# Kernel optimization log

Measured on AMD Instinct MI355X. Metric: run time of the kernel, lower is better.

Reference implementation:

```python
import jax, jax.numpy as jnp
import numpy as np

SIZE = 128   # feature dim
N = 4096     # number of mesh nodes


def setup_inputs() -> dict:
    key = jax.random.key(0)
    k_f, k_adj, k_q, k_k = jax.random.split(key, 4)
    # f: [size, N] node features (features-first, as in the torch module); scaled
    # so QK dot products stay O(1) and exp() is numerically safe.
    f = jax.random.normal(k_f, (SIZE, N), dtype=jnp.float32) * 0.1
    # neighbors: [N, N] binary adjacency with self-loops (every row sums > 0).
    adj = (jax.random.uniform(k_adj, (N, N)) < 0.005).astype(jnp.float32)
    neighbors = jnp.maximum(adj, jnp.eye(N, dtype=jnp.float32))
    # learned per-feature scale vectors (nn.init.normal_)
    wq = jax.random.normal(k_q, (SIZE,), dtype=jnp.float32)
    wk = jax.random.normal(k_k, (SIZE,), dtype=jnp.float32)
    return {"f": f, "neighbors": neighbors, "wq": wq, "wk": wk}


def reference(f, neighbors, wq, wk):
    # elementwise-scaled queries/keys: [size, N]
    wq_f = wq[:, None] * f
    wk_f = wk[:, None] * f
    # S[i, j] = exp(<wq_f[:, i], wk_f[:, j]>)  -> [N, N]
    S = jnp.exp(jnp.einsum('dn,dm->nm', wq_f, wk_f))
    # normalize by neighbor-sums: S / (neighbors @ S).T
    S = S / jnp.matmul(neighbors, S).T
    return S
```

## Files before the change

kernel.cpp:

```cpp
#include <hip/hip_runtime.h>
#include <hip/hip_fp16.h>

#define N     4096
#define SIZE  128
#define CAP   128
#define NMAX  120
#define RB    16
#define TB    1024

typedef __attribute__((ext_vector_type(8))) _Float16 f16x8;
typedef __attribute__((ext_vector_type(2))) __fp16 fp16x2;
typedef __attribute__((ext_vector_type(4))) float f32x4;

__device__ __forceinline__ unsigned int pk2(float lo, float hi) {
    union { fp16x2 v; unsigned int u; } c;
    c.v = __builtin_amdgcn_cvt_pkrtz(lo, hi);
    return c.u;
}
__device__ __forceinline__ __half2 u2h(unsigned int u) {
    union { unsigned int u; __half2 h; } c; c.u = u; return c.h;
}

__global__ __launch_bounds__(256)
void setup(const float* __restrict__ nb, const float* __restrict__ f,
           const float* __restrict__ wq, const float* __restrict__ wk,
           int* __restrict__ cnt, int* __restrict__ idx,
           _Float16* __restrict__ Af, _Float16* __restrict__ Bf) {
    __shared__ float sf[SIZE][16];
    __shared__ float sqw[SIZE];
    const int t = threadIdx.x;

    if (blockIdx.x < N / 4) {
        const int lane = t & 63;
        const int wv   = t >> 6;
        const int j    = blockIdx.x * 4 + wv;
        const float4* row4 = (const float4*)(nb + (size_t)j * N);
        int* irow = idx + (size_t)j * CAP;

        float4 v[16];
#pragma unroll
        for (int s = 0; s < 16; ++s) v[s] = row4[s * 64 + lane];

        unsigned long long m = 0ull;
#pragma unroll
        for (int s = 0; s < 16; ++s) {
            const float e[4] = {v[s].x, v[s].y, v[s].z, v[s].w};
#pragma unroll
            for (int q = 0; q < 4; ++q)
                if (e[q] != 0.0f) m |= 1ull << (s * 4 + q);
        }
        if (((j >> 2) & 63) == lane) m &= ~(1ull << ((j >> 8) * 4 + (j & 3)));

        const int pc = __popcll(m);
        int scan = pc;
#pragma unroll
        for (int s = 1; s < 64; s <<= 1) {
            const int o = __shfl_up(scan, s);
            if (lane >= s) scan += o;
        }
        int p = scan - pc;
        unsigned long long mm = m;
        while (mm) {
            const int b = __ffsll(mm) - 1;
            mm &= mm - 1ull;
            const int c = 4 * ((b >> 2) * 64 + lane) + (b & 3);
            if (p < NMAX) irow[p] = c;
            ++p;
        }
        if (lane == 63) {
            int n = scan;
            if (n > NMAX) n = NMAX;
            const int n8 = (n + 7) & ~7;
            for (int q = n; q < n8 + 8; ++q) irow[q] = N;
            cnt[j] = n8 >> 3;
        }
    } else {
        const int tile = blockIdx.x - N / 4;
        if (t < SIZE) sqw[t] = wq[t] * wk[t];
        const int col0 = t & 15;
#pragma unroll
        for (int it = 0; it < 8; ++it) {
            const int k = (t >> 4) + it * 16;
            sf[k][col0] = f[(size_t)k * N + tile * 16 + col0];
        }
        __syncthreads();
        const int ks   = t >> 6;
        const int lane = t & 63;
        const int quad = lane >> 4;
        const int col  = lane & 15;
        f16x8 va, vb;
#pragma unroll
        for (int jj = 0; jj < 8; ++jj) {
            const int k = ks * 32 + quad * 8 + jj;
            const float v = sf[k][col];
            va[jj] = (_Float16)(sqw[k] * v);
            vb[jj] = (_Float16)v;
        }
        const size_t o = (size_t)(tile * 4 + ks) * 64 + lane;
        ((f16x8*)Af)[o] = va;
        ((f16x8*)Bf)[o] = vb;
    }
}

__global__ __launch_bounds__(TB, 4)
void fused(const _Float16* __restrict__ Af, const _Float16* __restrict__ Bf,
           const int* __restrict__ cnt, const int* __restrict__ idx,
           float* __restrict__ out) {
    __shared__ uint4 Sb[2 * N + 3];
    uint4* const sA = Sb;
    uint4* const sB = Sb + N + 2;
    const int t    = threadIdx.x;
    const int lane = t & 63;
    const int wv   = t >> 6;
    const int quad = lane >> 4;
    const int i0   = blockIdx.x * RB;

    if (t == 0) {
        sA[N] = make_uint4(0u, 0u, 0u, 0u);
        sB[N] = make_uint4(0u, 0u, 0u, 0u);
    }

    int cc = cnt[t];
    const int4* ir0 = (const int4*)(idx + (size_t)t * CAP);
    int4 ka = ir0[0];
    int4 kb = ir0[1];

    f16x8 af[4];
    const f16x8* Ap = (const f16x8*)Af + (size_t)blockIdx.x * 4 * 64;
#pragma unroll
    for (int ks = 0; ks < 4; ++ks) af[ks] = Ap[ks * 64 + lane];
    const f16x8* Bp = (const f16x8*)Bf;

#pragma unroll 4
    for (int ti = 0; ti < 16; ++ti) {
        const int nt = wv * 16 + ti;
        f32x4 acc = {0.f, 0.f, 0.f, 0.f};
#pragma unroll
        for (int ks = 0; ks < 4; ++ks) {
            const f16x8 bfrag = Bp[(size_t)(nt * 4 + ks) * 64 + lane];
            acc = __builtin_amdgcn_mfma_f32_16x16x32_f16(af[ks], bfrag, acc, 0, 0, 0);
        }
        const int j = nt * 16 + (lane & 15);
        uint2 pp;
        pp.x = pk2(__expf(acc[0]), __expf(acc[1]));
        pp.y = pk2(__expf(acc[2]), __expf(acc[3]));
        uint2* bs = (quad < 2) ? (uint2*)&sA[j] : (uint2*)&sB[j];
        bs[quad & 1] = pp;
    }
    __syncthreads();

#define ACC(D, A, B) \
    D[0] = __hadd2(D[0], u2h((A).x)); D[1] = __hadd2(D[1], u2h((A).y)); \
    D[2] = __hadd2(D[2], u2h((A).z)); D[3] = __hadd2(D[3], u2h((A).w)); \
    D[4] = __hadd2(D[4], u2h((B).x)); D[5] = __hadd2(D[5], u2h((B).y)); \
    D[6] = __hadd2(D[6], u2h((B).z)); D[7] = __hadd2(D[7], u2h((B).w));

    for (int u = 0; u < 4; ++u) {
        const int j = t + u * TB;
        const int4* ir = (const int4*)(idx + (size_t)j * CAP);
        int ncc = 0; int4 nk0 = ka, nk1 = kb;
        if (u < 3) {
            const int jn = j + TB;
            const int4* irn = (const int4*)(idx + (size_t)jn * CAP);
            ncc = cnt[jn];
            nk0 = irn[0];
            nk1 = irn[1];
        }
        __half2 d0[8], d1[8], d2[8], d3[8];
        const __half2 z = u2h(0u);
#pragma unroll
        for (int r = 0; r < 8; ++r) { d0[r] = z; d1[r] = z; d2[r] = z; d3[r] = z; }

        for (int c = 0; c < cc; ++c) {
            const int4 pa = ir[2 * c + 2];
            const int4 pb = ir[2 * c + 3];
            const uint4 ax = sA[ka.x], bx = sB[ka.x];
            const uint4 ay = sA[ka.y], by = sB[ka.y];
            const uint4 az = sA[ka.z], bz = sB[ka.z];
            const uint4 aw = sA[ka.w], bw = sB[ka.w];
            const uint4 ex = sA[kb.x], fx = sB[kb.x];
            const uint4 ey = sA[kb.y], fy = sB[kb.y];
            const uint4 ez = sA[kb.z], fz = sB[kb.z];
            const uint4 ew = sA[kb.w], fw = sB[kb.w];
            ACC(d0, ax, bx)
            ACC(d1, ay, by)
            ACC(d0, az, bz)
            ACC(d1, aw, bw)
            ACC(d2, ex, fx)
            ACC(d3, ey, fy)
            ACC(d2, ez, fz)
            ACC(d3, ew, fw)
            ka = pa; kb = pb;
        }
        const uint4 na4 = sA[j], nb4 = sB[j];
        const unsigned int nu[8] = {na4.x, na4.y, na4.z, na4.w,
                                    nb4.x, nb4.y, nb4.z, nb4.w};
#pragma unroll
        for (int i = 0; i < 8; ++i) {
            const __half2 nn = u2h(nu[i]);
            __half2 dd = __hadd2(__hadd2(d0[i], d1[i]), __hadd2(d2[i], d3[i]));
            dd = __hadd2(dd, nn);
            out[(size_t)(i0 + 2 * i + 0) * N + j] =
                __low2float(nn)  * __builtin_amdgcn_rcpf(__low2float(dd));
            out[(size_t)(i0 + 2 * i + 1) * N + j] =
                __high2float(nn) * __builtin_amdgcn_rcpf(__high2float(dd));
        }
        cc = ncc; ka = nk0; kb = nk1;
    }
#undef ACC
}

extern "C" void kernel_launch(void* const* d_in, const int* in_sizes, int n_in,
                              void* d_out, int out_size, void* d_ws, size_t ws_size,
                              hipStream_t stream) {
    const float* f  = (const float*)d_in[0];
    const float* nb = (const float*)d_in[1];
    const float* wq = (const float*)d_in[2];
    const float* wk = (const float*)d_in[3];
    float* out = (float*)d_out;

    int*      cnt = (int*)d_ws;
    int*      idx = cnt + N;
    _Float16* Af  = (_Float16*)(idx + (size_t)N * CAP);
    _Float16* Bf  = Af + (size_t)256 * 4 * 64 * 8;

    setup<<<N / 4 + 256, 256, 0, stream>>>(nb, f, wq, wk, cnt, idx, Af, Bf);
    fused<<<N / RB, TB, 0, stream>>>(Af, Bf, cnt, idx, out);
}
```

Measured before the change: 147.8 us.

## Sort columns by neighbor count per block to balance wave loop trip counts

Adds an in-block counting sort that reorders the 4096 columns within each 1024-column group by neighbor-chunk count, using ballots and shared-memory prefix sums. Each thread then processes the permuted column, so lanes in a wave run similar gather-loop lengths and warp divergence in the neighbor-sum loop drops. The cost is an extra prologue with several block barriers and more shared memory. The output stores also become scattered across columns instead of coalesced, on what is likely the dominant memory traffic.

Result: slower. 183.9 us (+24.4%).

```diff
diff --git a/kernel.cpp b/kernel.cpp
--- a/kernel.cpp
+++ b/kernel.cpp
@@ -107,6 +107,9 @@
            const int* __restrict__ cnt, const int* __restrict__ idx,
            float* __restrict__ out) {
     __shared__ uint4 Sb[2 * N + 3];
+    __shared__ int   sperm[4][1024];
+    __shared__ int   wcnt[4][16][16];
+    __shared__ int   bbase[4][16];
     uint4* const sA = Sb;
     uint4* const sB = Sb + N + 2;
     const int t    = threadIdx.x;
@@ -114,14 +117,61 @@
     const int wv   = t >> 6;
     const int quad = lane >> 4;
     const int i0   = blockIdx.x * RB;
+    const unsigned long long ltm = (1ull << lane) - 1ull;
+
+    int cj[4], within[4];
+#pragma unroll
+    for (int g = 0; g < 4; ++g) cj[g] = cnt[g * 1024 + t];
+#pragma unroll
+    for (int g = 0; g < 4; ++g) {
+        within[g] = 0;
+        for (int bb = 0; bb < 16; ++bb) {
+            const unsigned long long mk = __ballot(cj[g] == bb);
+            if (cj[g] == bb) within[g] = __popcll(mk & ltm);
+            if (lane == bb) wcnt[g][wv][bb] = __popcll(mk);
+        }
+    }
+    __syncthreads();
+    if (t < 64) {
+        const int g = t >> 4, b = t & 15;
+        int s = 0;
+#pragma unroll
+        for (int w = 0; w < 16; ++w) {
+            const int tmp = wcnt[g][w][b];
+            wcnt[g][w][b] = s;
+            s += tmp;
+        }
+        bbase[g][b] = s;
+    }
+    __syncthreads();
+    if (t < 4) {
+        const int g = t;
+        int s = 0;
+#pragma unroll
+        for (int b = 0; b < 16; ++b) {
+            const int tmp = bbase[g][b];
+            bbase[g][b] = s;
+            s += tmp;
+        }
+    }
+    __syncthreads();
+#pragma unroll
+    for (int g = 0; g < 4; ++g) {
+        const int rank = bbase[g][cj[g]] + wcnt[g][wv][cj[g]] + within[g];
+        sperm[g][rank] = (g * 1024 + t) | (cj[g] << 12);
+    }
+    __syncthreads();
+    int myperm[4];
+#pragma unroll
+    for (int g = 0; g < 4; ++g) myperm[g] = sperm[g][t];
 
     if (t == 0) {
         sA[N] = make_uint4(0u, 0u, 0u, 0u);
         sB[N] = make_uint4(0u, 0u, 0u, 0u);
     }
 
-    int cc = cnt[t];
-    const int4* ir0 = (const int4*)(idx + (size_t)t * CAP);
+    int cc = myperm[0] >> 12;
+    const int4* ir0 = (const int4*)(idx + (size_t)(myperm[0] & 4095) * CAP);
     int4 ka = ir0[0];
     int4 kb = ir0[1];
 
@@ -156,16 +206,14 @@
     D[6] = __hadd2(D[6], u2h((B).z)); D[7] = __hadd2(D[7], u2h((B).w));
 
     for (int u = 0; u < 4; ++u) {
-        const int j = t + u * TB;
+        const int j = myperm[u] & 4095;
         const int4* ir = (const int4*)(idx + (size_t)j * CAP);
-        int ncc = 0; int4 nk0 = ka, nk1 = kb;
-        if (u < 3) {
-            const int jn = j + TB;
-            const int4* irn = (const int4*)(idx + (size_t)jn * CAP);
-            ncc = cnt[jn];
-            nk0 = irn[0];
-            nk1 = irn[1];
-        }
+        const int pn = (u < 3) ? myperm[u + 1] : myperm[u];
+        const int4* irn = (const int4*)(idx + (size_t)(pn & 4095) * CAP);
+        const int  ncc = pn >> 12;
+        const int4 nk0 = irn[0];
+        const int4 nk1 = irn[1];
+
         __half2 d0[8], d1[8], d2[8], d3[8];
         const __half2 z = u2h(0u);
 #pragma unroll
```
